# Kernel tuning notes

Hardware: AMD Instinct MI355X
Metric: run time of the kernel (lower is better)

Reference implementation:

```python
import jax, jax.numpy as jnp
import numpy as np

B, C_H, C_L = 8, 128, 256
H_H, W_H = 64, 64
H_L, W_L = 128, 128
CS = 8
K = CS * CS  # 64 external keys (== inter_channels, matches hardcoded reatt dim)
EPS = 1e-5


def _bn(x, g, b, m, v):
    # inference-mode BatchNorm2d over channel dim 1
    scale = g / jnp.sqrt(v + EPS)
    return (x - m[None, :, None, None]) * scale[None, :, None, None] + b[None, :, None, None]


def setup_inputs() -> dict:
    key = jax.random.key(0)
    ks = jax.random.split(key, 13)
    return {
        "x_h": jax.random.normal(ks[0], (B, C_H, H_H, W_H), jnp.float32),
        "x_l": jax.random.normal(ks[1], (B, C_L, H_L, W_L), jnp.float32),
        "bn_h_gamma": jax.random.normal(ks[2], (C_H,), jnp.float32),
        "bn_h_beta": jax.random.normal(ks[3], (C_H,), jnp.float32),
        "bn_h_mean": jax.random.normal(ks[4], (C_H,), jnp.float32),
        "bn_h_var": jax.random.uniform(ks[5], (C_H,), jnp.float32),
        "kv_w": jax.random.normal(ks[6], (2 * C_L, C_H), jnp.float32) * 0.05,
        "kv_b": jax.random.normal(ks[7], (2 * C_L,), jnp.float32) * 0.05,
        "bn_l_gamma": jax.random.normal(ks[8], (C_L,), jnp.float32),
        "bn_l_beta": jax.random.normal(ks[9], (C_L,), jnp.float32),
        "bn_l_mean": jax.random.normal(ks[10], (C_L,), jnp.float32),
        "bn_l_var": jax.random.uniform(ks[11], (C_L,), jnp.float32),
        "reatt": jax.random.normal(ks[12], (1, K, 1, 1), jnp.float32) * 1e-5,
    }


def reference(x_h, x_l, bn_h_gamma, bn_h_beta, bn_h_mean, bn_h_var,
              kv_w, kv_b, bn_l_gamma, bn_l_beta, bn_l_mean, bn_l_var, reatt):
    # ---- cross_kv: BN -> AdaptiveMaxPool2d(8,8) -> 1x1 conv ----
    xh = _bn(x_h, bn_h_gamma, bn_h_beta, bn_h_mean, bn_h_var)
    # exact window max pool (H_H, W_H divisible by CS)
    p = xh.reshape(B, C_H, CS, H_H // CS, CS, W_H // CS).max(axis=(3, 5))  # [B,C_H,8,8]
    kv = jnp.einsum('bchw,oc->bohw', p, kv_w) + kv_b[None, :, None, None]  # [B,2*C_L,8,8]
    ck = kv[:, :C_L]   # [B,C_L,8,8]
    cv = kv[:, C_L:]   # [B,C_L,8,8]
    # cross_k: permute NHWC then flatten -> per-sample [K, C_L] key matrix
    ck = ck.transpose(0, 2, 3, 1).reshape(B, K, C_L)
    # cross_v: flatten spatial -> per-sample [C_L, K] value matrix
    cv = cv.reshape(B, C_L, K)

    # ---- ExternalAttention (use_cross_kv path) ----
    xl = _bn(x_l, bn_l_gamma, bn_l_beta, bn_l_mean, bn_l_var)
    # grouped 1x1 conv (groups=B) == per-sample projection onto K external keys
    attn = jnp.einsum('bchw,bkc->bkhw', xl, ck)          # [B,K,H_L,W_L]
    attn = attn + reatt                                   # broadcast [1,K,1,1]
    # _act_sn: scale by inter_channels^-0.5, softmax over the K key channels
    attn = jax.nn.softmax(attn * (K ** -0.5), axis=1)
    # grouped 1x1 conv with values: per-sample [C_L,K] @ [K,H*W]
    out = jnp.einsum('bkhw,bck->bchw', attn, cv)          # [B,C_L,H_L,W_L]
    return x_l + out
```

## Files before the change

### kernel.cpp

```cpp
#include <hip/hip_runtime.h>
#include <math.h>

#define B_     8
#define C_H_   128
#define C_L_   256
#define K_     64
#define NPIX_L 16384
#define EPS_   1e-5f

#define P_OFF     0
#define P_SZ      (B_*K_*C_H_)
#define B1_BYTE   (P_SZ*4)
#define B2_BYTE   (B1_BYTE + B_*K_*C_L_*2)
#define BIAS_BYTE (B2_BYTE + B_*K_*C_L_*2)

typedef short bf16x8 __attribute__((ext_vector_type(8)));
typedef float f32x4  __attribute__((ext_vector_type(4)));

__device__ inline unsigned short f2bf(float f) {
    unsigned int u = __float_as_uint(f);
    u += 0x7FFFu + ((u >> 16) & 1u);
    return (unsigned short)(u >> 16);
}
__device__ inline unsigned int pack2bf(float lo, float hi) {
    unsigned int ul = __float_as_uint(lo);
    unsigned int uh = __float_as_uint(hi);
    ul = (ul + (0x7FFFu + ((ul >> 16) & 1u))) >> 16;
    uh = (uh + (0x7FFFu + ((uh >> 16) & 1u))) & 0xFFFF0000u;
    return ul | uh;
}

#define MFMA16(a, b, c) __builtin_amdgcn_mfma_f32_16x16x32_bf16((a), (b), (c), 0, 0, 0)

__global__ __launch_bounds__(256) void pool_bn_kernel(
    const float* __restrict__ x_h,
    const float* __restrict__ g, const float* __restrict__ be,
    const float* __restrict__ mn, const float* __restrict__ vr,
    float* __restrict__ ws)
{
    const int t   = threadIdx.x;
    const int k   = t & 63;
    const int cl  = t >> 6;
    const int bid = blockIdx.x;
    const int b   = bid >> 5;
    const int c   = ((bid & 31) << 2) + cl;

    const float* plane = x_h + ((size_t)(b * C_H_ + c) << 12);
    const int ph = k >> 3, pw = k & 7;
    const float* p0 = plane + (ph * 8) * 64 + pw * 8;

    float mx = -INFINITY, mnv = INFINITY;
#pragma unroll
    for (int i = 0; i < 8; i++) {
        const float4 a  = *reinterpret_cast<const float4*>(p0 + i * 64);
        const float4 bq = *reinterpret_cast<const float4*>(p0 + i * 64 + 4);
        mx  = fmaxf(mx,  fmaxf(fmaxf(a.x, a.y),  fmaxf(a.z, a.w)));
        mx  = fmaxf(mx,  fmaxf(fmaxf(bq.x, bq.y), fmaxf(bq.z, bq.w)));
        mnv = fminf(mnv, fminf(fminf(a.x, a.y),  fminf(a.z, a.w)));
        mnv = fminf(mnv, fminf(fminf(bq.x, bq.y), fminf(bq.z, bq.w)));
    }
    const float sc  = g[c] * rsqrtf(vr[c] + EPS_);
    const float sel = (sc >= 0.f) ? mx : mnv;
    ws[P_OFF + (b * K_ + k) * C_H_ + c] = fmaf(sel - mn[c], sc, be[c]);
}

__global__ __launch_bounds__(256) void kv_kernel(
    const float* __restrict__ kv_w, const float* __restrict__ kv_b,
    const float* __restrict__ lg, const float* __restrict__ lb,
    const float* __restrict__ lm, const float* __restrict__ lv,
    const float* __restrict__ ratt,
    float* __restrict__ ws)
{
    __shared__ __align__(16) float prow[C_H_];
    __shared__ float red[4];
    const int t   = threadIdx.x;
    const int bid = blockIdx.x;
    const int b   = bid >> 6;
    const int kk  = bid & 63;

    if (t < C_H_ / 4) {
        reinterpret_cast<float4*>(prow)[t] =
            reinterpret_cast<const float4*>(ws + P_OFF + (b * K_ + kk) * C_H_)[t];
    }
    __syncthreads();

    float a0 = kv_b[t];
    float a1 = kv_b[t + 256];
    const float* w0 = kv_w + (size_t)t * C_H_;
    const float* w1 = kv_w + (size_t)(t + 256) * C_H_;
#pragma unroll
    for (int c = 0; c < C_H_; c += 4) {
        const float4 pv  = *reinterpret_cast<const float4*>(prow + c);
        const float4 wv0 = *reinterpret_cast<const float4*>(w0 + c);
        const float4 wv1 = *reinterpret_cast<const float4*>(w1 + c);
        a0 = fmaf(wv0.x, pv.x, a0); a0 = fmaf(wv0.y, pv.y, a0);
        a0 = fmaf(wv0.z, pv.z, a0); a0 = fmaf(wv0.w, pv.w, a0);
        a1 = fmaf(wv1.x, pv.x, a1); a1 = fmaf(wv1.y, pv.y, a1);
        a1 = fmaf(wv1.z, pv.z, a1); a1 = fmaf(wv1.w, pv.w, a1);
    }

    const float s = lg[t] * rsqrtf(lv[t] + EPS_);
    const float h = fmaf(-lm[t], s, lb[t]);

    float contrib = h * a0;
#pragma unroll
    for (int m = 1; m < 64; m <<= 1) contrib += __shfl_xor(contrib, m, 64);
    if ((t & 63) == 0) red[t >> 6] = contrib;
    __syncthreads();

    unsigned short* b1 = (unsigned short*)((char*)ws + B1_BYTE);
    unsigned short* b2 = (unsigned short*)((char*)ws + B2_BYTE);

    {
        const int s1 = t >> 5, j = t & 7;
        const int l  = ((t >> 3) & 3) * 16 + (kk & 15);
        const int n  = kk >> 4;
        b1[((((b * 8 + s1) * 4 + n) * 64) + l) * 8 + j] = f2bf(a0 * s);
    }
    {
        const int s2 = kk >> 5, j2 = kk & 7;
        const int l2 = ((kk >> 3) & 3) * 16 + (t & 15);
        const int n2 = t >> 4;
        b2[((((b * 2 + s2) * 16 + n2) * 64) + l2) * 8 + j2] = f2bf(a1);
    }
    if (t == 0) {
        float* bia = (float*)((char*)ws + BIAS_BYTE);
        bia[b * K_ + kk] = (red[0] + red[1] + red[2] + red[3] + ratt[kk]) * 0.125f;
    }
}

__global__ __launch_bounds__(256, 4) void attn_mfma(
    const float* __restrict__ x_l,
    const float* __restrict__ ws_f,
    float* __restrict__ out)
{
    __shared__ unsigned short wa[128 * 72];

    const int t    = threadIdx.x;
    const int lane = t & 63;
    const int wid  = t >> 6;
    const int bid  = blockIdx.x;
    const int b    = bid & 7;
    const int tile = bid >> 3;
    const int pw0  = tile * 128 + wid * 32;
    const int r16  = lane & 15;
    const int q    = lane >> 4;

    const unsigned short* b1 = (const unsigned short*)((const char*)ws_f + B1_BYTE);
    const unsigned short* b2 = (const unsigned short*)((const char*)ws_f + B2_BYTE);
    const float* biasf = (const float*)((const char*)ws_f + BIAS_BYTE) + b * K_;
    const float* xb = x_l + (size_t)b * (C_L_ * NPIX_L);

    float bl[4];
#pragma unroll
    for (int n = 0; n < 4; n++) bl[n] = biasf[16 * n + r16];

    f32x4 acc1[2][4] = {};
    union ABu { bf16x8 v; unsigned int u[4]; };
    const float* xpx = xb + pw0 + r16;

#pragma unroll
    for (int s = 0; s < 8; s++) {
        const int c0 = 32 * s + q * 8;
        float xv0[8], xv1[8];
#pragma unroll
        for (int j = 0; j < 8; j++) {
            xv0[j] = xpx[(size_t)(c0 + j) * NPIX_L];
            xv1[j] = xpx[(size_t)(c0 + j) * NPIX_L + 16];
        }
        ABu a0f, a1f;
#pragma unroll
        for (int jj = 0; jj < 4; jj++) {
            a0f.u[jj] = pack2bf(xv0[2 * jj], xv0[2 * jj + 1]);
            a1f.u[jj] = pack2bf(xv1[2 * jj], xv1[2 * jj + 1]);
        }
        const bf16x8* bp = ((const bf16x8*)b1) + ((b * 8 + s) * 4) * 64 + lane;
#pragma unroll
        for (int n = 0; n < 4; n++) {
            const bf16x8 bfr = bp[n * 64];
            acc1[0][n] = MFMA16(a0f.v, bfr, acc1[0][n]);
            acc1[1][n] = MFMA16(a1f.v, bfr, acc1[1][n]);
        }
    }

    const int plbase = wid * 32;
#pragma unroll
    for (int m = 0; m < 2; m++) {
#pragma unroll
        for (int r = 0; r < 4; r++) {
            float e0 = fmaf(acc1[m][0][r], 0.125f, bl[0]);
            float e1 = fmaf(acc1[m][1][r], 0.125f, bl[1]);
            float e2 = fmaf(acc1[m][2][r], 0.125f, bl[2]);
            float e3 = fmaf(acc1[m][3][r], 0.125f, bl[3]);
            float mx = fmaxf(fmaxf(e0, e1), fmaxf(e2, e3));
#pragma unroll
            for (int msk = 1; msk < 16; msk <<= 1) mx = fmaxf(mx, __shfl_xor(mx, msk, 64));
            e0 = __expf(e0 - mx); e1 = __expf(e1 - mx);
            e2 = __expf(e2 - mx); e3 = __expf(e3 - mx);
            float sm = (e0 + e1) + (e2 + e3);
#pragma unroll
            for (int msk = 1; msk < 16; msk <<= 1) sm += __shfl_xor(sm, msk, 64);
            const float inv = 1.f / sm;
            unsigned short* wp = wa + (plbase + 16 * m + q * 4 + r) * 72 + r16;
            wp[0]  = f2bf(e0 * inv);
            wp[16] = f2bf(e1 * inv);
            wp[32] = f2bf(e2 * inv);
            wp[48] = f2bf(e3 * inv);
        }
    }

    bf16x8 af[2][2];
#pragma unroll
    for (int m = 0; m < 2; m++)
#pragma unroll
        for (int s = 0; s < 2; s++)
            af[m][s] = *(const bf16x8*)(wa + (plbase + 16 * m + r16) * 72 + 32 * s + q * 8);

    float* ob = out + (size_t)b * (C_L_ * NPIX_L);
#pragma unroll
    for (int nc = 0; nc < 4; nc++) {
        f32x4 acc2[2][4] = {};
#pragma unroll
        for (int s = 0; s < 2; s++) {
            const bf16x8* bp2 = ((const bf16x8*)b2) + ((b * 2 + s) * 16 + nc * 4) * 64 + lane;
#pragma unroll
            for (int nn = 0; nn < 4; nn++) {
                const bf16x8 bfr = bp2[nn * 64];
                acc2[0][nn] = MFMA16(af[0][s], bfr, acc2[0][nn]);
                acc2[1][nn] = MFMA16(af[1][s], bfr, acc2[1][nn]);
            }
        }
#pragma unroll
        for (int m = 0; m < 2; m++) {
#pragma unroll
            for (int nn = 0; nn < 4; nn++) {
                const int co = 16 * (nc * 4 + nn) + r16;
                const size_t base = (size_t)co * NPIX_L + pw0 + 16 * m + q * 4;
#pragma unroll
                for (int r = 0; r < 4; r++) {
                    ob[base + r] = acc2[m][nn][r] + xb[base + r];
                }
            }
        }
    }
}

extern "C" void kernel_launch(void* const* d_in, const int* in_sizes, int n_in,
                              void* d_out, int out_size, void* d_ws, size_t ws_size,
                              hipStream_t stream) {
    const float* x_h  = (const float*)d_in[0];
    const float* x_l  = (const float*)d_in[1];
    const float* hg   = (const float*)d_in[2];
    const float* hb   = (const float*)d_in[3];
    const float* hm   = (const float*)d_in[4];
    const float* hv   = (const float*)d_in[5];
    const float* kvw  = (const float*)d_in[6];
    const float* kvb  = (const float*)d_in[7];
    const float* lg   = (const float*)d_in[8];
    const float* lb   = (const float*)d_in[9];
    const float* lm   = (const float*)d_in[10];
    const float* lv   = (const float*)d_in[11];
    const float* ratt = (const float*)d_in[12];
    float* ws  = (float*)d_ws;
    float* out = (float*)d_out;

    pool_bn_kernel<<<256, 256, 0, stream>>>(x_h, hg, hb, hm, hv, ws);
    kv_kernel<<<512, 256, 0, stream>>>(kvw, kvb, lg, lb, lm, lv, ratt, ws);
    attn_mfma<<<1024, 256, 0, stream>>>(x_l, ws, out);
}
```

Baseline: 331.3 us.

## Stage x_l tiles via async global-to-LDS loads and coalesce output stores through LDS

Replaces the per-thread strided scalar loads of x_l in the first GEMM with double-buffered global_load_lds DMA into a swizzled shared buffer, so each channel row is fetched as 16-byte coalesced chunks and the next stage overlaps with the MFMAs. The softmax scratch becomes per-wave, which removes the need for a cross-wave barrier. Output tiles are staged through LDS and written together with the residual add as float4 row-contiguous stores, instead of scattered scalar stores. The cost is more barriers, larger LDS use (about 33KB, which may limit occupancy at 4 blocks per CU), and hand-written waitcnt dependencies that could be fragile.

Result: faster. 306.6 us (-7.5%).

```diff
diff --git a/kernel.cpp b/kernel.cpp
--- a/kernel.cpp
+++ b/kernel.cpp
@@ -31,6 +31,10 @@
 }
 
 #define MFMA16(a, b, c) __builtin_amdgcn_mfma_f32_16x16x32_bf16((a), (b), (c), 0, 0, 0)
+
+#define GLOAD_LDS16(g, l) __builtin_amdgcn_global_load_lds( \
+    (const __attribute__((address_space(1))) void*)(g), \
+    (__attribute__((address_space(3))) void*)(l), 16, 0, 0)
 
 __global__ __launch_bounds__(256) void pool_bn_kernel(
     const float* __restrict__ x_h,
@@ -134,7 +138,11 @@
     const float* __restrict__ ws_f,
     float* __restrict__ out)
 {
-    __shared__ unsigned short wa[128 * 72];
+    __shared__ __align__(16) char lds[33280];
+    float* xbuf0 = (float*)lds;
+    float* xbuf1 = (float*)(lds + 16384);
+    unsigned short* wscr = (unsigned short*)lds;
+    float* obuf = (float*)(lds + 16384);
 
     const int t    = threadIdx.x;
     const int lane = t & 63;
@@ -142,7 +150,8 @@
     const int bid  = blockIdx.x;
     const int b    = bid & 7;
     const int tile = bid >> 3;
-    const int pw0  = tile * 128 + wid * 32;
+    const int px0  = tile * 128;
+    const int pxw  = wid * 32;
     const int r16  = lane & 15;
     const int q    = lane >> 4;
 
@@ -150,29 +159,49 @@
     const unsigned short* b2 = (const unsigned short*)((const char*)ws_f + B2_BYTE);
     const float* biasf = (const float*)((const char*)ws_f + BIAS_BYTE) + b * K_;
     const float* xb = x_l + (size_t)b * (C_L_ * NPIX_L);
+    float* ob = out + (size_t)b * (C_L_ * NPIX_L);
 
     float bl[4];
 #pragma unroll
     for (int n = 0; n < 4; n++) bl[n] = biasf[16 * n + r16];
+
+    const int su = ((lane & 31) ^ (wid << 2)) << 2;
+    const int sd = lane >> 5;
+#define STAGE(bufp, s_) do { \
+    _Pragma("unroll") \
+    for (int i_ = 0; i_ < 4; i_++) { \
+        const int cl_ = 8 * wid + 2 * i_; \
+        const float* gp_ = xb + (size_t)(32 * (s_) + cl_ + sd) * NPIX_L + px0 + su; \
+        GLOAD_LDS16(gp_, (bufp) + (size_t)cl_ * 128); \
+    } \
+} while (0)
 
     f32x4 acc1[2][4] = {};
     union ABu { bf16x8 v; unsigned int u[4]; };
-    const float* xpx = xb + pw0 + r16;
+
+    STAGE(xbuf0, 0);
+
+    const int p0x = (pxw + r16) ^ (q << 4);
+    const int p1x = (pxw + 16 + r16) ^ (q << 4);
 
 #pragma unroll
     for (int s = 0; s < 8; s++) {
-        const int c0 = 32 * s + q * 8;
-        float xv0[8], xv1[8];
-#pragma unroll
-        for (int j = 0; j < 8; j++) {
-            xv0[j] = xpx[(size_t)(c0 + j) * NPIX_L];
-            xv1[j] = xpx[(size_t)(c0 + j) * NPIX_L + 16];
-        }
+        float* xbf = (s & 1) ? xbuf1 : xbuf0;
+        if (s < 7) {
+            STAGE((s & 1) ? xbuf0 : xbuf1, s + 1);
+            asm volatile("s_waitcnt vmcnt(4)" ::: "memory");
+        } else {
+            asm volatile("s_waitcnt vmcnt(0)" ::: "memory");
+        }
+        __builtin_amdgcn_s_barrier();
+
         ABu a0f, a1f;
 #pragma unroll
         for (int jj = 0; jj < 4; jj++) {
-            a0f.u[jj] = pack2bf(xv0[2 * jj], xv0[2 * jj + 1]);
-            a1f.u[jj] = pack2bf(xv1[2 * jj], xv1[2 * jj + 1]);
+            const float* row0 = xbf + (8 * q + 2 * jj) * 128;
+            const float* row1 = xbf + (8 * q + 2 * jj + 1) * 128;
+            a0f.u[jj] = pack2bf(row0[p0x], row1[p0x]);
+            a1f.u[jj] = pack2bf(row0[p1x], row1[p1x]);
         }
         const bf16x8* bp = ((const bf16x8*)b1) + ((b * 8 + s) * 4) * 64 + lane;
 #pragma unroll
@@ -181,9 +210,11 @@
             acc1[0][n] = MFMA16(a0f.v, bfr, acc1[0][n]);
             acc1[1][n] = MFMA16(a1f.v, bfr, acc1[1][n]);
         }
-    }
-
-    const int plbase = wid * 32;
+        __builtin_amdgcn_s_barrier();
+    }
+
+    unsigned short* wsb = wscr + wid * 1152;
+    bf16x8 af[2][2];
 #pragma unroll
     for (int m = 0; m < 2; m++) {
 #pragma unroll
@@ -201,48 +232,60 @@
 #pragma unroll
             for (int msk = 1; msk < 16; msk <<= 1) sm += __shfl_xor(sm, msk, 64);
             const float inv = 1.f / sm;
-            unsigned short* wp = wa + (plbase + 16 * m + q * 4 + r) * 72 + r16;
+            unsigned short* wp = wsb + (q * 4 + r) * 72 + r16;
             wp[0]  = f2bf(e0 * inv);
             wp[16] = f2bf(e1 * inv);
             wp[32] = f2bf(e2 * inv);
             wp[48] = f2bf(e3 * inv);
         }
-    }
-
-    bf16x8 af[2][2];
-#pragma unroll
-    for (int m = 0; m < 2; m++)
-#pragma unroll
-        for (int s = 0; s < 2; s++)
-            af[m][s] = *(const bf16x8*)(wa + (plbase + 16 * m + r16) * 72 + 32 * s + q * 8);
-
-    float* ob = out + (size_t)b * (C_L_ * NPIX_L);
+#pragma unroll
+        for (int s2 = 0; s2 < 2; s2++)
+            af[m][s2] = *(const bf16x8*)(wsb + r16 * 72 + 32 * s2 + q * 8);
+        if (m == 0) asm volatile("s_waitcnt lgkmcnt(0)" ::: "memory");
+    }
+
 #pragma unroll
     for (int nc = 0; nc < 4; nc++) {
         f32x4 acc2[2][4] = {};
 #pragma unroll
-        for (int s = 0; s < 2; s++) {
-            const bf16x8* bp2 = ((const bf16x8*)b2) + ((b * 2 + s) * 16 + nc * 4) * 64 + lane;
+        for (int s2 = 0; s2 < 2; s2++) {
+            const bf16x8* bp2 = ((const bf16x8*)b2) + ((b * 2 + s2) * 16 + nc * 4) * 64 + lane;
 #pragma unroll
             for (int nn = 0; nn < 4; nn++) {
                 const bf16x8 bfr = bp2[nn * 64];
-                acc2[0][nn] = MFMA16(af[0][s], bfr, acc2[0][nn]);
-                acc2[1][nn] = MFMA16(af[1][s], bfr, acc2[1][nn]);
+                acc2[0][nn] = MFMA16(af[0][s2], bfr, acc2[0][nn]);
+                acc2[1][nn] = MFMA16(af[1][s2], bfr, acc2[1][nn]);
             }
         }
 #pragma unroll
-        for (int m = 0; m < 2; m++) {
-#pragma unroll
-            for (int nn = 0; nn < 4; nn++) {
-                const int co = 16 * (nc * 4 + nn) + r16;
-                const size_t base = (size_t)co * NPIX_L + pw0 + 16 * m + q * 4;
-#pragma unroll
-                for (int r = 0; r < 4; r++) {
-                    ob[base + r] = acc2[m][nn][r] + xb[base + r];
+        for (int h = 0; h < 2; h++) {
+#pragma unroll
+            for (int m = 0; m < 2; m++)
+#pragma unroll
+                for (int e = 0; e < 2; e++) {
+                    float* dp = obuf + (16 * e + r16) * 132 + (pxw + 16 * m + 4 * q);
+                    *(f32x4*)dp = acc2[m][2 * h + e];
                 }
+            asm volatile("s_waitcnt lgkmcnt(0)" ::: "memory");
+            __builtin_amdgcn_s_barrier();
+            const int cbase = 64 * nc + 32 * h;
+#pragma unroll
+            for (int u2 = 0; u2 < 4; u2++) {
+                const int idx = t + 256 * u2;
+                const int col = idx >> 5;
+                const int un  = idx & 31;
+                const float4 vv = *(const float4*)(obuf + col * 132 + un * 4);
+                const size_t gbase = (size_t)(cbase + col) * NPIX_L + px0 + un * 4;
+                const float4 xv4 = *(const float4*)(xb + gbase);
+                float4 o;
+                o.x = vv.x + xv4.x; o.y = vv.y + xv4.y;
+                o.z = vv.z + xv4.z; o.w = vv.w + xv4.w;
+                *(float4*)(ob + gbase) = o;
             }
-        }
-    }
+            __builtin_amdgcn_s_barrier();
+        }
+    }
+#undef STAGE
 }
 
 extern "C" void kernel_launch(void* const* d_in, const int* in_sizes, int n_in,
```
